# Optimization experiments

Measured on AMD Instinct MI355X. Metric: run time of the kernel, lower is better.

The kernel has to match this reference:

```python
import jax, jax.numpy as jnp
import numpy as np

DEPTH_CHANNEL = 48  # max_disp(192) / downsample_scale(4)


def setup_inputs() -> dict:
    key = jax.random.key(0)
    k1, k2 = jax.random.split(key)
    B, C, H, W = 4, 512, 96, 312
    left_features = jax.random.normal(k1, (B, C, H, W), dtype=jnp.float32)
    right_features = jax.random.normal(k2, (B, C, H, W), dtype=jnp.float32)
    return {"left_features": left_features, "right_features": right_features}


def reference(left_features, right_features):
    # PSM cosine cost volume: for each disparity i,
    #   cost[:, i, :, i:] = mean_c(left[:, :, :, i:] * right[:, :, :, :W-i])
    # positions w < i remain zero (from the pre-zeroed tensor in the original).
    B, C, H, W = left_features.shape
    planes = []
    for i in range(DEPTH_CHANNEL):  # small fixed disparity loop (48), unrolled under jit
        corr = jnp.mean(
            left_features[:, :, :, i:] * right_features[:, :, :, : W - i],
            axis=1,
        )  # [B, H, W-i]
        planes.append(jnp.pad(corr, ((0, 0), (0, 0), (i, 0))))  # zero-fill w < i
    return jnp.stack(planes, axis=1)  # [B, D, H, W]
```

## Files before the change

### kernel.cpp

```cpp
#include <hip/hip_runtime.h>
#include <hip/hip_bf16.h>
#include <stdint.h>


#define B_ 4
#define C_ 512
#define H_ 96
#define W_ 312
#define D_ 48
#define HW_ (H_ * W_)
#define CHW_ (C_ * HW_)

#define KC 64
#define NCHUNK (C_ / KC)
#define HALFW 156
#define LCOLS 160
#define RCOLS 208
#define PITCH 128
#define LBYTES (LCOLS * PITCH)
#define RBYTES (RCOLS * PITCH)
#define SMEM_BYTES (LBYTES + RBYTES)

typedef __bf16 bf16x8 __attribute__((ext_vector_type(8)));
typedef float  f32x4  __attribute__((ext_vector_type(4)));

__device__ __forceinline__ uint32_t pack2_bf16(float a, float b) {
    uint32_t ua = __builtin_bit_cast(uint32_t, a);
    uint32_t ub = __builtin_bit_cast(uint32_t, b);
    ua += 0x7FFFu + ((ua >> 16) & 1u);
    ub += 0x7FFFu + ((ub >> 16) & 1u);
    return (ua >> 16) | (ub & 0xFFFF0000u);
}

__device__ __forceinline__ int lds_slotoff(int lw, int chi) {
    return lw * PITCH + ((chi ^ (lw & 7) ^ ((lw >> 4) & 7)) << 4);
}

__global__ __launch_bounds__(512, 4)
void psm_cost_volume(const float* __restrict__ lf,
                     const float* __restrict__ rf,
                     float* __restrict__ out) {
    const int half = blockIdx.x;
    const int h    = blockIdx.y;
    const int b    = blockIdx.z;
    const int wb   = half * HALFW;
    const int tid  = threadIdx.x;
    const int lane = tid & 63;
    const int wave = tid >> 6;
    const int l15  = lane & 15;
    const int l4   = lane >> 4;
    const int jj   = wave & 3;
    const int nb   = wave >> 2;

    extern __shared__ char smem[];

    const float* lbase = lf + (size_t)b * CHW_ + (size_t)h * W_;
    const float* rbase = rf + (size_t)b * CHW_ + (size_t)h * W_;

    f32x4 acc[5];
    #pragma unroll
    for (int i = 0; i < 5; ++i) acc[i] = f32x4{0.f, 0.f, 0.f, 0.f};

    for (int ch = 0; ch < NCHUNK; ++ch) {
        const int c0 = ch * KC;
        if (ch) __syncthreads();

        #pragma unroll
        for (int it = 0; it < 3; ++it) {
            int idx = tid + it * 512;
            if (idx < 32 * 40) {
                int rp = idx / 40;
                int q  = idx - rp * 40;
                int w4 = wb + 4 * q;
                f32x4 v0 = {0.f, 0.f, 0.f, 0.f}, v1 = {0.f, 0.f, 0.f, 0.f};
                if (w4 + 3 < W_) {
                    const float* g = lbase + (size_t)(c0 + 2 * rp) * HW_ + w4;
                    v0 = *(const f32x4*)g;
                    v1 = *(const f32x4*)(g + HW_);
                }
                const int chi = rp >> 2;
                const int cb  = (rp & 3) << 2;
                #pragma unroll
                for (int j = 0; j < 4; ++j) {
                    int lw = 4 * q + j;
                    *(uint32_t*)(smem + lds_slotoff(lw, chi) + cb) =
                        pack2_bf16(v0[j], v1[j]);
                }
            }
        }
        #pragma unroll
        for (int it = 0; it < 4; ++it) {
            int idx = tid + it * 512;
            if (idx < 32 * 52) {
                int rp = idx / 52;
                int q  = idx - rp * 52;
                int w4 = wb - 48 + 4 * q;
                f32x4 v0 = {0.f, 0.f, 0.f, 0.f}, v1 = {0.f, 0.f, 0.f, 0.f};
                if (w4 >= 0 && w4 + 3 < W_) {
                    const float* g = rbase + (size_t)(c0 + 2 * rp) * HW_ + w4;
                    v0 = *(const f32x4*)g;
                    v1 = *(const f32x4*)(g + HW_);
                }
                const int chi = rp >> 2;
                const int cb  = (rp & 3) << 2;
                #pragma unroll
                for (int j = 0; j < 4; ++j) {
                    int lw = 4 * q + j;
                    *(uint32_t*)(smem + LBYTES + lds_slotoff(lw, chi) + cb) =
                        pack2_bf16(v0[j], v1[j]);
                }
            }
        }
        __syncthreads();

        #pragma unroll
        for (int ks = 0; ks < 2; ++ks) {
            const int chi = ks * 4 + l4;
            #pragma unroll
            for (int pi = 0; pi < 5; ++pi) {
                const int n   = 2 * pi + nb;
                const int lwB = 16 * n + l15;
                const int lwA = 16 * (n + jj) + l15;
                bf16x8 bfrag = *(const bf16x8*)(smem + lds_slotoff(lwB, chi));
                bf16x8 afrag = *(const bf16x8*)(smem + LBYTES + lds_slotoff(lwA, chi));
                acc[pi] = __builtin_amdgcn_mfma_f32_16x16x32_bf16(afrag, bfrag, acc[pi], 0, 0, 0);
            }
        }
    }
    __syncthreads();

    float* outs = (float*)smem;
    #pragma unroll
    for (int pi = 0; pi < 5; ++pi) {
        const int n  = 2 * pi + nb;
        const int lw = 16 * n + l15;
        #pragma unroll
        for (int r = 0; r < 4; ++r) {
            int tm = 4 * l4 + r;
            int d  = 48 - 16 * jj + l15 - tm;
            if (d >= 0 && d < D_ && lw < HALFW) {
                outs[d * HALFW + lw] = acc[pi][r] * (1.f / 512.f);
            }
        }
    }
    __syncthreads();

    float* obase = out + (size_t)b * (D_ * HW_) + (size_t)h * W_ + wb;
    for (int idx = tid; idx < D_ * HALFW; idx += 512) {
        int d  = idx / HALFW;
        int lw = idx - d * HALFW;
        obase[(size_t)d * HW_ + lw] = outs[idx];
    }
}

extern "C" void kernel_launch(void* const* d_in, const int* in_sizes, int n_in,
                              void* d_out, int out_size, void* d_ws, size_t ws_size,
                              hipStream_t stream) {
    const float* lf = (const float*)d_in[0];
    const float* rf = (const float*)d_in[1];
    float* out = (float*)d_out;
    dim3 grid(2, H_, B_);
    psm_cost_volume<<<grid, 512, SMEM_BYTES, stream>>>(lf, rf, out);
}
```

Baseline: 121.8 us.

## Prefetch next channel chunk into registers while computing current chunk

Global loads for the next channel chunk are issued into registers right after the current chunk is written to LDS. They are converted and stored to LDS on the following iteration, so global memory latency overlaps the MFMA work and the barriers. The cost is about 56 extra VGPRs for the prefetch buffers, which may reduce occupancy under the 512-thread, 4-block launch bounds or cause spills.

```diff
diff --git a/kernel.cpp b/kernel.cpp
--- a/kernel.cpp
+++ b/kernel.cpp
@@ -20,6 +20,9 @@
 #define LBYTES (LCOLS * PITCH)
 #define RBYTES (RCOLS * PITCH)
 #define SMEM_BYTES (LBYTES + RBYTES)
+
+#define LITEMS 3
+#define RITEMS 4
 
 typedef __bf16 bf16x8 __attribute__((ext_vector_type(8)));
 typedef float  f32x4  __attribute__((ext_vector_type(4)));
@@ -61,56 +64,83 @@
     #pragma unroll
     for (int i = 0; i < 5; ++i) acc[i] = f32x4{0.f, 0.f, 0.f, 0.f};
 
-    for (int ch = 0; ch < NCHUNK; ++ch) {
-        const int c0 = ch * KC;
-        if (ch) __syncthreads();
+    f32x4 pl0[LITEMS], pl1[LITEMS], pr0[RITEMS], pr1[RITEMS];
 
+    auto LOADS = [&](int c0) {
         #pragma unroll
-        for (int it = 0; it < 3; ++it) {
+        for (int it = 0; it < LITEMS; ++it) {
             int idx = tid + it * 512;
             if (idx < 32 * 40) {
                 int rp = idx / 40;
                 int q  = idx - rp * 40;
                 int w4 = wb + 4 * q;
-                f32x4 v0 = {0.f, 0.f, 0.f, 0.f}, v1 = {0.f, 0.f, 0.f, 0.f};
+                pl0[it] = f32x4{0.f, 0.f, 0.f, 0.f};
+                pl1[it] = f32x4{0.f, 0.f, 0.f, 0.f};
                 if (w4 + 3 < W_) {
                     const float* g = lbase + (size_t)(c0 + 2 * rp) * HW_ + w4;
-                    v0 = *(const f32x4*)g;
-                    v1 = *(const f32x4*)(g + HW_);
-                }
-                const int chi = rp >> 2;
-                const int cb  = (rp & 3) << 2;
-                #pragma unroll
-                for (int j = 0; j < 4; ++j) {
-                    int lw = 4 * q + j;
-                    *(uint32_t*)(smem + lds_slotoff(lw, chi) + cb) =
-                        pack2_bf16(v0[j], v1[j]);
+                    pl0[it] = *(const f32x4*)g;
+                    pl1[it] = *(const f32x4*)(g + HW_);
                 }
             }
         }
         #pragma unroll
-        for (int it = 0; it < 4; ++it) {
+        for (int it = 0; it < RITEMS; ++it) {
             int idx = tid + it * 512;
             if (idx < 32 * 52) {
                 int rp = idx / 52;
                 int q  = idx - rp * 52;
                 int w4 = wb - 48 + 4 * q;
-                f32x4 v0 = {0.f, 0.f, 0.f, 0.f}, v1 = {0.f, 0.f, 0.f, 0.f};
+                pr0[it] = f32x4{0.f, 0.f, 0.f, 0.f};
+                pr1[it] = f32x4{0.f, 0.f, 0.f, 0.f};
                 if (w4 >= 0 && w4 + 3 < W_) {
                     const float* g = rbase + (size_t)(c0 + 2 * rp) * HW_ + w4;
-                    v0 = *(const f32x4*)g;
-                    v1 = *(const f32x4*)(g + HW_);
+                    pr0[it] = *(const f32x4*)g;
+                    pr1[it] = *(const f32x4*)(g + HW_);
                 }
-                const int chi = rp >> 2;
-                const int cb  = (rp & 3) << 2;
+            }
+        }
+    };
+
+    auto WRITES = [&]() {
+        #pragma unroll
+        for (int it = 0; it < LITEMS; ++it) {
+            int idx = tid + it * 512;
+            if (idx < 32 * 40) {
+                int rp  = idx / 40;
+                int q   = idx - rp * 40;
+                int chi = rp >> 2;
+                int cb  = (rp & 3) << 2;
+                #pragma unroll
+                for (int j = 0; j < 4; ++j) {
+                    int lw = 4 * q + j;
+                    *(uint32_t*)(smem + lds_slotoff(lw, chi) + cb) =
+                        pack2_bf16(pl0[it][j], pl1[it][j]);
+                }
+            }
+        }
+        #pragma unroll
+        for (int it = 0; it < RITEMS; ++it) {
+            int idx = tid + it * 512;
+            if (idx < 32 * 52) {
+                int rp  = idx / 52;
+                int q   = idx - rp * 52;
+                int chi = rp >> 2;
+                int cb  = (rp & 3) << 2;
                 #pragma unroll
                 for (int j = 0; j < 4; ++j) {
                     int lw = 4 * q + j;
                     *(uint32_t*)(smem + LBYTES + lds_slotoff(lw, chi) + cb) =
-                        pack2_bf16(v0[j], v1[j]);
+                        pack2_bf16(pr0[it][j], pr1[it][j]);
                 }
             }
         }
+    };
+
+    LOADS(0);
+    for (int ch = 0; ch < NCHUNK; ++ch) {
+        if (ch) __syncthreads();
+        WRITES();
+        if (ch + 1 < NCHUNK) LOADS((ch + 1) * KC);
         __syncthreads();
 
         #pragma unroll
```

After: 192.9 us. 58.3% more time.
